# Kernel optimization log

Hardware: AMD Instinct MI355X
Metric: run time of the kernel (lower is better)

## Reference

```python
import jax, jax.numpy as jnp
import numpy as np

N = 50000        # nodes
E = 800000       # edges (avg degree 16)
F = 64           # in/out feature dim (scatter into zeros_like(x) forces out==in)
H = 128          # hidden dim
CIN = 2 * F + 1  # combined_features dim


def setup_inputs() -> dict:
    key = jax.random.key(0)
    ks = jax.random.split(key, 12)
    x = jax.random.normal(ks[0], (N, F), dtype=jnp.float32)
    pos = jax.random.normal(ks[1], (N, 3), dtype=jnp.float32)
    edge_index = jax.random.randint(ks[2], (2, E), 0, N, dtype=jnp.int64)
    s1 = 1.0 / np.sqrt(CIN)
    s2 = 1.0 / np.sqrt(H)
    W1x = jax.random.uniform(ks[3], (CIN, H), jnp.float32, -s1, s1)
    b1x = jax.random.uniform(ks[4], (H,), jnp.float32, -s1, s1)
    W2x = jax.random.uniform(ks[5], (H, F), jnp.float32, -s2, s2)
    b2x = jax.random.uniform(ks[6], (F,), jnp.float32, -s2, s2)
    W1p = jax.random.uniform(ks[7], (CIN, H), jnp.float32, -s1, s1)
    b1p = jax.random.uniform(ks[8], (H,), jnp.float32, -s1, s1)
    W2p = jax.random.uniform(ks[9], (H, 1), jnp.float32, -s2, s2)
    b2p = jax.random.uniform(ks[10], (1,), jnp.float32, -s2, s2)
    return {"x": x, "pos": pos, "edge_index": edge_index,
            "W1x": W1x, "b1x": b1x, "W2x": W2x, "b2x": b2x,
            "W1p": W1p, "b1p": b1p, "W2p": W2p, "b2p": b2p}


def reference(x, pos, edge_index, W1x, b1x, W2x, b2x, W1p, b1p, W2p, b2p):
    row, col = edge_index[0], edge_index[1]
    rel_pos = pos[row] - pos[col]                              # [E, 3]
    dist_sq = jnp.sum(rel_pos * rel_pos, axis=-1, keepdims=True)  # [E, 1]
    combined = jnp.concatenate([x[row], x[col], dist_sq], axis=-1)  # [E, 2F+1]
    # phi_x: Linear -> SiLU -> Linear
    msg_x = jax.nn.silu(combined @ W1x + b1x) @ W2x + b2x      # [E, F]
    aggregated_x = jax.ops.segment_sum(msg_x, col, num_segments=x.shape[0])
    # phi_pos: Linear -> SiLU -> Linear (scalar weight per edge)
    weight_pos = jax.nn.silu(combined @ W1p + b1p) @ W2p + b2p  # [E, 1]
    pos_update = weight_pos * rel_pos                           # [E, 3]
    aggregated_pos = jax.ops.segment_sum(pos_update, col, num_segments=pos.shape[0])
    return aggregated_x, aggregated_pos
```

## Files before the change

### kernel.cpp

```cpp
#include <hip/hip_runtime.h>

typedef short short8 __attribute__((ext_vector_type(8)));
typedef float floatx4 __attribute__((ext_vector_type(4)));

__device__ __forceinline__ unsigned short f2bf(float f) {
  unsigned int u = __float_as_uint(f);
  u += 0x7FFFu + ((u >> 16) & 1u);
  return (unsigned short)(u >> 16);
}

#if __has_builtin(__builtin_amdgcn_cvt_pk_bf16_f32)
typedef __bf16 bf16x2_t __attribute__((ext_vector_type(2)));
__device__ __forceinline__ unsigned int pk2bf(float lo, float hi) {
  bf16x2_t v = __builtin_amdgcn_cvt_pk_bf16_f32(lo, hi);
  return __builtin_bit_cast(unsigned int, v);
}
#else
__device__ __forceinline__ unsigned int pk2bf(float lo, float hi) {
  return (unsigned)f2bf(lo) | ((unsigned)f2bf(hi) << 16);
}
#endif

__device__ __forceinline__ float silu(float h) {
  return h * __builtin_amdgcn_rcpf(1.f + __expf(-h));
}

__global__ __launch_bounds__(256) void k_mega(
    float* __restrict__ out, int out_n,
    const int* __restrict__ colp, int E, int* __restrict__ hist,
    const float* __restrict__ x, int N,
    const float* __restrict__ W1x, const float* __restrict__ W1p,
    const float* __restrict__ W2x,
    const float* __restrict__ b1x, const float* __restrict__ b1p,
    unsigned short* __restrict__ wbuf,
    unsigned int* __restrict__ Ar, unsigned int* __restrict__ Ac,
    int b1, int b2, int b3)
{
  __shared__ __align__(16) unsigned short xt[64][72];
  const int blk = blockIdx.x, t = threadIdx.x;

  if (blk < b1) {
    const int n0 = blk * 64;
    const int wv = t >> 6, lane = t & 63, quad = lane >> 4, lc = lane & 15;

    {
      int nd = t >> 2, p = t & 3;
      int n = n0 + nd;
      uint4 o0, o1;
      if (n < N) {
        const float4* xp = (const float4*)(x + (size_t)n*64 + p*16);
        float4 a = xp[0], b = xp[1], c = xp[2], d = xp[3];
        o0 = make_uint4(pk2bf(a.x,a.y), pk2bf(a.z,a.w), pk2bf(b.x,b.y), pk2bf(b.z,b.w));
        o1 = make_uint4(pk2bf(c.x,c.y), pk2bf(c.z,c.w), pk2bf(d.x,d.y), pk2bf(d.z,d.w));
      } else {
        o0 = o1 = make_uint4(0u,0u,0u,0u);
      }
      *(uint4*)&xt[nd][p*16]     = o0;
      *(uint4*)&xt[nd][p*16 + 8] = o1;
    }

    short8 fxr[2][2], fxc[2][2], fpr[2][2], fpc[2][2];
    float bxv[2][4], bpv[2][4];
    #pragma unroll
    for (int ti = 0; ti < 2; ++ti) {
      const int nt = wv + 4*ti;
      const int n  = nt*16 + lc;
      #pragma unroll
      for (int k2 = 0; k2 < 2; ++k2) {
        #pragma unroll
        for (int j = 0; j < 8; ++j) {
          const int kr = k2*32 + quad*8 + j;
          fxr[ti][k2][j] = (short)f2bf(W1x[kr*128 + n]);
          fxc[ti][k2][j] = (short)f2bf(W1x[(64 + kr)*128 + n]);
          fpr[ti][k2][j] = (short)f2bf(W1p[kr*128 + n]);
          fpc[ti][k2][j] = (short)f2bf(W1p[(64 + kr)*128 + n]);
        }
      }
      #pragma unroll
      for (int r = 0; r < 4; ++r) {
        bxv[ti][r] = b1x[nt*16 + quad*4 + r];
        bpv[ti][r] = b1p[nt*16 + quad*4 + r];
      }
    }
    __syncthreads();

    #pragma unroll 1
    for (int mw = 0; mw < 4; ++mw) {
      short8 bb0 = *(const short8*)&xt[mw*16 + lc][quad*8];
      short8 bb1 = *(const short8*)&xt[mw*16 + lc][32 + quad*8];
      const int nd = n0 + mw*16 + lc;
      #pragma unroll
      for (int ti = 0; ti < 2; ++ti) {
        floatx4 xr = {0,0,0,0}, xc = {0,0,0,0}, pr = {0,0,0,0}, pc = {0,0,0,0};
        xr = __builtin_amdgcn_mfma_f32_16x16x32_bf16(fxr[ti][0], bb0, xr, 0,0,0);
        xr = __builtin_amdgcn_mfma_f32_16x16x32_bf16(fxr[ti][1], bb1, xr, 0,0,0);
        xc = __builtin_amdgcn_mfma_f32_16x16x32_bf16(fxc[ti][0], bb0, xc, 0,0,0);
        xc = __builtin_amdgcn_mfma_f32_16x16x32_bf16(fxc[ti][1], bb1, xc, 0,0,0);
        pr = __builtin_amdgcn_mfma_f32_16x16x32_bf16(fpr[ti][0], bb0, pr, 0,0,0);
        pr = __builtin_amdgcn_mfma_f32_16x16x32_bf16(fpr[ti][1], bb1, pr, 0,0,0);
        pc = __builtin_amdgcn_mfma_f32_16x16x32_bf16(fpc[ti][0], bb0, pc, 0,0,0);
        pc = __builtin_amdgcn_mfma_f32_16x16x32_bf16(fpc[ti][1], bb1, pc, 0,0,0);
        if (nd < N) {
          const int hbase = (wv + 4*ti)*16 + quad*4;
          uint4 ur = make_uint4(pk2bf(xr[0]+bxv[ti][0], pr[0]+bpv[ti][0]),
                                pk2bf(xr[1]+bxv[ti][1], pr[1]+bpv[ti][1]),
                                pk2bf(xr[2]+bxv[ti][2], pr[2]+bpv[ti][2]),
                                pk2bf(xr[3]+bxv[ti][3], pr[3]+bpv[ti][3]));
          uint4 uc = make_uint4(pk2bf(xc[0], pc[0]), pk2bf(xc[1], pc[1]),
                                pk2bf(xc[2], pc[2]), pk2bf(xc[3], pc[3]));
          *(uint4*)(Ar + (size_t)nd*128 + hbase) = ur;
          *(uint4*)(Ac + (size_t)nd*128 + hbase) = uc;
        }
      }
    }
  } else if (blk < b2) {
    int i = ((blk - b1) * 256 + t) * 16;
    #pragma unroll
    for (int q = 0; q < 4; ++q) {
      int j = i + q*4;
      if (j + 4 <= out_n) *(float4*)(out + j) = make_float4(0.f,0.f,0.f,0.f);
      else for (int k = j; k < out_n; ++k) out[k] = 0.f;
    }
  } else if (blk < b3) {
    int i4 = (blk - b2) * 256 + t;
    if (i4 < (E >> 2)) {
      int4 c = *(const int4*)(colp + i4*4);
      atomicAdd(&hist[c.x], 1); atomicAdd(&hist[c.y], 1);
      atomicAdd(&hist[c.z], 1); atomicAdd(&hist[c.w], 1);
    }
    if (blk == b2 && t == 0)
      for (int k = E & ~3; k < E; ++k) atomicAdd(&hist[colp[k]], 1);
  } else {
    int i = (blk - b3) * 256 + t;
    if (i < 8192) {
      int jj = i & 7, lane = (i >> 3) & 63, ks = (i >> 9) & 3, nt = (i >> 11) & 3;
      int k = ks*32 + (lane >> 4)*8 + jj;
      wbuf[i] = f2bf(W2x[k*64 + nt*16 + (lane & 15)]);
    }
  }
}

__global__ __launch_bounds__(256) void k_scan_a(
    int* __restrict__ hist, int N, int* __restrict__ bsum) {
  __shared__ int wtot[4], wexc[4];
  int t = threadIdx.x, lane = t & 63, w = t >> 6;
  int base = blockIdx.x * 1024 + t * 4;
  int v0 = (base + 0 < N) ? hist[base + 0] : 0;
  int v1 = (base + 1 < N) ? hist[base + 1] : 0;
  int v2 = (base + 2 < N) ? hist[base + 2] : 0;
  int v3 = (base + 3 < N) ? hist[base + 3] : 0;
  int T = v0 + v1 + v2 + v3;
  int inc = T;
  #pragma unroll
  for (int s = 1; s < 64; s <<= 1) {
    int u = __shfl_up(inc, s, 64);
    if (lane >= s) inc += u;
  }
  if (lane == 63) wtot[w] = inc;
  __syncthreads();
  if (t == 0) {
    int a = 0;
    #pragma unroll
    for (int i = 0; i < 4; ++i) { wexc[i] = a; a += wtot[i]; }
    bsum[blockIdx.x] = a;
  }
  __syncthreads();
  int tex = wexc[w] + (inc - T);
  if (base + 0 < N) hist[base + 0] = tex;
  if (base + 1 < N) hist[base + 1] = tex + v0;
  if (base + 2 < N) hist[base + 2] = tex + v0 + v1;
  if (base + 3 < N) hist[base + 3] = tex + v0 + v1 + v2;
}

__global__ __launch_bounds__(256) void k_scatter(
    const int* __restrict__ row, const int* __restrict__ col, int E,
    int* __restrict__ excl, const int* __restrict__ bsum, int NB,
    int2* __restrict__ sedge) {
  __shared__ int boff_sh[64];
  int t = threadIdx.x;
  if (t < 64) {
    int v = (t < NB) ? bsum[t] : 0;
    int inc = v;
    #pragma unroll
    for (int s = 1; s < 64; s <<= 1) {
      int u = __shfl_up(inc, s, 64);
      if (t >= s) inc += u;
    }
    boff_sh[t] = inc - v;
  }
  __syncthreads();
  int i4 = blockIdx.x * 256 + t;
  if (i4 < (E >> 2)) {
    int4 c = *(const int4*)(col + i4*4);
    int4 r = *(const int4*)(row + i4*4);
    int p;
    p = atomicAdd(&excl[c.x], 1) + boff_sh[c.x >> 10]; sedge[p] = make_int2(r.x, c.x);
    p = atomicAdd(&excl[c.y], 1) + boff_sh[c.y >> 10]; sedge[p] = make_int2(r.y, c.y);
    p = atomicAdd(&excl[c.z], 1) + boff_sh[c.z >> 10]; sedge[p] = make_int2(r.z, c.z);
    p = atomicAdd(&excl[c.w], 1) + boff_sh[c.w >> 10]; sedge[p] = make_int2(r.w, c.w);
  }
  if (blockIdx.x == 0 && t == 0) {
    for (int k = E & ~3; k < E; ++k) {
      int c = col[k];
      int p = atomicAdd(&excl[c], 1) + boff_sh[c >> 10];
      sedge[p] = make_int2(row[k], c);
    }
  }
}

__global__ __launch_bounds__(256) void mp_main(
    const float* __restrict__ pos,
    const int2* __restrict__ sedge, int E,
    const unsigned int* __restrict__ Ar, const unsigned int* __restrict__ Ac,
    const float* __restrict__ W1x, const float* __restrict__ W1p,
    const float* __restrict__ b2x, const float* __restrict__ W2p,
    const float* __restrict__ b2p,
    const unsigned short* __restrict__ wbuf,
    float* __restrict__ out_x, float* __restrict__ out_pos)
{
  __shared__ __align__(16) unsigned short H_lds[64][136];
  __shared__ __align__(16) uint4 edata[64];
  __shared__ float rel_lds[64][3];
  __shared__ int   col_sh[64];
  __shared__ float wsum[4][64];

  const int t    = threadIdx.x;
  const int e0   = blockIdx.x * 64;
  const int wv   = t >> 6;
  const int lane = t & 63;
  const int quad = lane >> 4;
  const int lc   = lane & 15;

  if (t < 64) {
    int e = e0 + t;
    int r = 0, c = 0, cs = -1;
    float rp0 = 0.f, rp1 = 0.f, rp2 = 0.f, dsq = 0.f;
    if (e < E) {
      int2 rc = sedge[e]; r = rc.x; c = rc.y;
      cs = c;
      float pr0 = pos[r*3+0], pr1 = pos[r*3+1], pr2 = pos[r*3+2];
      float pc0 = pos[c*3+0], pc1 = pos[c*3+1], pc2 = pos[c*3+2];
      rp0 = pr0 - pc0; rp1 = pr1 - pc1; rp2 = pr2 - pc2;
      dsq = rp0*rp0 + rp1*rp1 + rp2*rp2;
    }
    rel_lds[t][0] = rp0; rel_lds[t][1] = rp1; rel_lds[t][2] = rp2;
    col_sh[t] = cs;
    edata[t] = make_uint4((unsigned)r, (unsigned)c, __float_as_uint(dsq), 0u);
  }

  const short8* __restrict__ w2x_f = (const short8*)wbuf;
  short8 a2w[4];
  #pragma unroll
  for (int ks = 0; ks < 4; ++ks) a2w[ks] = w2x_f[(wv*4 + ks)*64 + lane];

  float w1xd[2][4], w1pd[2][4], wp2[2][4], b2xr[4];
  #pragma unroll
  for (int ti = 0; ti < 2; ++ti)
    #pragma unroll
    for (int r = 0; r < 4; ++r) {
      int h = (wv + 4*ti)*16 + quad*4 + r;
      w1xd[ti][r] = W1x[16384 + h];
      w1pd[ti][r] = W1p[16384 + h];
      wp2[ti][r]  = W2p[h];
    }
  #pragma unroll
  for (int r = 0; r < 4; ++r) b2xr[r] = b2x[wv*16 + quad*4 + r];
  const float b2ps = b2p[0];
  __syncthreads();

  #pragma unroll 2
  for (int et = 0; et < 4; ++et) {
    uint4 ed = edata[et*16 + lc];
    const float dsqv = __uint_as_float(ed.z);
    float ps = 0.f;
    #pragma unroll
    for (int ti = 0; ti < 2; ++ti) {
      const int ht = wv + 4*ti;
      const int hb = ht*32 + quad*8;
      uint4 va = *(const uint4*)((const unsigned short*)Ar + (size_t)ed.x*256 + hb);
      uint4 vc = *(const uint4*)((const unsigned short*)Ac + (size_t)ed.y*256 + hb);
      float sx[4];
      #pragma unroll
      for (int j = 0; j < 4; ++j) {
        unsigned a = (&va.x)[j], bb = (&vc.x)[j];
        float hx = __uint_as_float(a << 16) + __uint_as_float(bb << 16)
                 + dsqv * w1xd[ti][j];
        float hp = __uint_as_float(a & 0xffff0000u) + __uint_as_float(bb & 0xffff0000u)
                 + dsqv * w1pd[ti][j];
        sx[j] = silu(hx);
        ps += silu(hp) * wp2[ti][j];
      }
      *(uint2*)&H_lds[et*16 + lc][ht*16 + quad*4] =
          make_uint2(pk2bf(sx[0], sx[1]), pk2bf(sx[2], sx[3]));
    }
    ps += __shfl_xor(ps, 16, 64);
    ps += __shfl_xor(ps, 32, 64);
    if (lane < 16) wsum[wv][et*16 + lane] = ps;
  }
  __syncthreads();

  #pragma unroll 2
  for (int et = 0; et < 4; ++et) {
    floatx4 acc = {0,0,0,0};
    #pragma unroll
    for (int ks = 0; ks < 4; ++ks) {
      short8 b = *(const short8*)&H_lds[et*16 + lc][ks*32 + quad*8];
      acc = __builtin_amdgcn_mfma_f32_16x16x32_bf16(a2w[ks], b, acc, 0, 0, 0);
    }
    int edge = et*16 + lc;
    int myc = col_sh[edge];
    float v0 = acc[0] + b2xr[0], v1 = acc[1] + b2xr[1];
    float v2 = acc[2] + b2xr[2], v3 = acc[3] + b2xr[3];
    #pragma unroll
    for (int s = 1; s < 16; s <<= 1) {
      int   nc = __shfl_down(myc, s, 64);
      float n0 = __shfl_down(v0,  s, 64);
      float n1 = __shfl_down(v1,  s, 64);
      float n2 = __shfl_down(v2,  s, 64);
      float n3 = __shfl_down(v3,  s, 64);
      if ((lc + s < 16) && (nc == myc)) { v0 += n0; v1 += n1; v2 += n2; v3 += n3; }
    }
    bool head = (myc >= 0) && (lc == 0 || col_sh[edge-1] != myc);
    if (head) {
      float* dst = out_x + (size_t)myc*64 + wv*16 + quad*4;
      atomicAdd(dst + 0, v0);
      atomicAdd(dst + 1, v1);
      atomicAdd(dst + 2, v2);
      atomicAdd(dst + 3, v3);
    }
  }

  if (t < 64) {
    int c = col_sh[t];
    float w = wsum[0][t] + wsum[1][t] + wsum[2][t] + wsum[3][t] + b2ps;
    float p0 = w * rel_lds[t][0], p1 = w * rel_lds[t][1], p2 = w * rel_lds[t][2];
    #pragma unroll
    for (int s = 1; s < 64; s <<= 1) {
      int   nc = __shfl_down(c,  s, 64);
      float n0 = __shfl_down(p0, s, 64);
      float n1 = __shfl_down(p1, s, 64);
      float n2 = __shfl_down(p2, s, 64);
      if ((t + s < 64) && (nc == c)) { p0 += n0; p1 += n1; p2 += n2; }
    }
    bool head = (c >= 0) && (t == 0 || col_sh[t-1] != c);
    if (head) {
      atomicAdd(&out_pos[(size_t)c*3 + 0], p0);
      atomicAdd(&out_pos[(size_t)c*3 + 1], p1);
      atomicAdd(&out_pos[(size_t)c*3 + 2], p2);
    }
  }
}

extern "C" void kernel_launch(void* const* d_in, const int* in_sizes, int n_in,
                              void* d_out, int out_size, void* d_ws, size_t ws_size,
                              hipStream_t stream) {
  const float* x   = (const float*)d_in[0];
  const float* pos = (const float*)d_in[1];
  const int*   ei  = (const int*)d_in[2];
  const float* W1x = (const float*)d_in[3];
  const float* b1x = (const float*)d_in[4];
  const float* W2x = (const float*)d_in[5];
  const float* b2x = (const float*)d_in[6];
  const float* W1p = (const float*)d_in[7];
  const float* b1p = (const float*)d_in[8];
  const float* W2p = (const float*)d_in[9];
  const float* b2p = (const float*)d_in[10];

  const int E = in_sizes[2] / 2;
  const int N = in_sizes[0] / 64;
  const int* rowp = ei;
  const int* colp = ei + E;
  float* out_x   = (float*)d_out;
  float* out_pos = out_x + (size_t)N * 64;
  const int NB = (N + 1023) / 1024;

  char* ws = (char*)d_ws;
  const size_t tab_one = (size_t)N * 512;
  unsigned int*   Ar   = (unsigned int*)ws;
  unsigned int*   Ac   = (unsigned int*)(ws + tab_one);
  unsigned short* wbuf = (unsigned short*)(ws + 2*tab_one);
  int*  hist  = (int*)(ws + 2*tab_one + 16384);
  int*  bsum  = (int*)(ws + 2*tab_one + 16384 + 200192);
  int2* sedge = (int2*)(ws + 2*tab_one + 16384 + 200192 + 512);

  hipMemsetAsync(hist, 0, (size_t)N * sizeof(int), stream);

  const int nb_node = (N + 63) / 64;
  const int nb_zero = (out_size + 4095) / 4096;
  const int nb_hist = ((E >> 2) + 255) / 256;
  const int nb_rep  = 32;
  const int b1 = nb_node, b2 = b1 + nb_zero, b3 = b2 + nb_hist;
  k_mega<<<b3 + nb_rep, 256, 0, stream>>>(
      (float*)d_out, out_size, colp, E, hist, x, N,
      W1x, W1p, W2x, b1x, b1p, wbuf, Ar, Ac, b1, b2, b3);

  k_scan_a<<<NB, 256, 0, stream>>>(hist, N, bsum);
  k_scatter<<<((E >> 2) + 255) / 256, 256, 0, stream>>>(
      rowp, colp, E, hist, bsum, NB, sedge);

  mp_main<<<(E + 63) / 64, 256, 0, stream>>>(
      pos, sedge, E, Ar, Ac, W1x, W1p, b2x, W2p, b2p, wbuf, out_x, out_pos);
}
```

Baseline: 311.9 us.

## Prefetch all gathered Ar/Ac rows upfront via wave shuffles, drop edata LDS and barrier

Every wave now loads its 64 edges' indices and positions redundantly, then broadcasts row, col and dist_sq with cross-lane shuffles instead of staging them in shared memory behind a barrier. All 16 uint4 gathers from Ar/Ac per thread are issued at once before the compute loop, so the loads can overlap with each other and with the weight loads. The intent is to hide gather latency and remove one __syncthreads. The cost is much higher register pressure (32 extra VGPR-wide uint4 values), which could lower occupancy, plus redundant index and position loads across the four waves.

```diff
diff --git a/kernel.cpp b/kernel.cpp
--- a/kernel.cpp
+++ b/kernel.cpp
@@ -219,7 +219,6 @@
     float* __restrict__ out_x, float* __restrict__ out_pos)
 {
   __shared__ __align__(16) unsigned short H_lds[64][136];
-  __shared__ __align__(16) uint4 edata[64];
   __shared__ float rel_lds[64][3];
   __shared__ int   col_sh[64];
   __shared__ float wsum[4][64];
@@ -231,21 +230,36 @@
   const int quad = lane >> 4;
   const int lc   = lane & 15;
 
-  if (t < 64) {
-    int e = e0 + t;
-    int r = 0, c = 0, cs = -1;
-    float rp0 = 0.f, rp1 = 0.f, rp2 = 0.f, dsq = 0.f;
+  int erow = 0, ecol = 0, cs = -1;
+  float dsq = 0.f, rp0 = 0.f, rp1 = 0.f, rp2 = 0.f;
+  {
+    int e = e0 + lane;
     if (e < E) {
-      int2 rc = sedge[e]; r = rc.x; c = rc.y;
-      cs = c;
-      float pr0 = pos[r*3+0], pr1 = pos[r*3+1], pr2 = pos[r*3+2];
-      float pc0 = pos[c*3+0], pc1 = pos[c*3+1], pc2 = pos[c*3+2];
+      int2 rc = sedge[e];
+      erow = rc.x; ecol = rc.y; cs = ecol;
+      float pr0 = pos[erow*3+0], pr1 = pos[erow*3+1], pr2 = pos[erow*3+2];
+      float pc0 = pos[ecol*3+0], pc1 = pos[ecol*3+1], pc2 = pos[ecol*3+2];
       rp0 = pr0 - pc0; rp1 = pr1 - pc1; rp2 = pr2 - pc2;
       dsq = rp0*rp0 + rp1*rp1 + rp2*rp2;
     }
+  }
+  if (t < 64) {
     rel_lds[t][0] = rp0; rel_lds[t][1] = rp1; rel_lds[t][2] = rp2;
     col_sh[t] = cs;
-    edata[t] = make_uint4((unsigned)r, (unsigned)c, __float_as_uint(dsq), 0u);
+  }
+
+  uint4 va[4][2], vc[4][2];
+  #pragma unroll
+  for (int et = 0; et < 4; ++et) {
+    const int src = et*16 + lc;
+    int r_et = __shfl(erow, src, 64);
+    int c_et = __shfl(ecol, src, 64);
+    #pragma unroll
+    for (int ti = 0; ti < 2; ++ti) {
+      const int hb = (wv + 4*ti)*32 + quad*8;
+      va[et][ti] = *(const uint4*)((const unsigned short*)Ar + (size_t)r_et*256 + hb);
+      vc[et][ti] = *(const uint4*)((const unsigned short*)Ac + (size_t)c_et*256 + hb);
+    }
   }
 
   const short8* __restrict__ w2x_f = (const short8*)wbuf;
@@ -266,23 +280,18 @@
   #pragma unroll
   for (int r = 0; r < 4; ++r) b2xr[r] = b2x[wv*16 + quad*4 + r];
   const float b2ps = b2p[0];
-  __syncthreads();
-
-  #pragma unroll 2
+
+  #pragma unroll
   for (int et = 0; et < 4; ++et) {
-    uint4 ed = edata[et*16 + lc];
-    const float dsqv = __uint_as_float(ed.z);
+    const float dsqv = __shfl(dsq, et*16 + lc, 64);
     float ps = 0.f;
     #pragma unroll
     for (int ti = 0; ti < 2; ++ti) {
       const int ht = wv + 4*ti;
-      const int hb = ht*32 + quad*8;
-      uint4 va = *(const uint4*)((const unsigned short*)Ar + (size_t)ed.x*256 + hb);
-      uint4 vc = *(const uint4*)((const unsigned short*)Ac + (size_t)ed.y*256 + hb);
       float sx[4];
       #pragma unroll
       for (int j = 0; j < 4; ++j) {
-        unsigned a = (&va.x)[j], bb = (&vc.x)[j];
+        unsigned a = (&va[et][ti].x)[j], bb = (&vc[et][ti].x)[j];
         float hx = __uint_as_float(a << 16) + __uint_as_float(bb << 16)
                  + dsqv * w1xd[ti][j];
         float hp = __uint_as_float(a & 0xffff0000u) + __uint_as_float(bb & 0xffff0000u)
```

After: 330.4 us. +6.0%, slower.

## Make each wave own 16 edges end to end, removing LDS staging and barriers

Applied to the files above, without the earlier changes.

The block's work is repartitioned so that each wavefront handles its own 16 edges through the whole pipeline: gather, first layer, SiLU, the MFMA second layer, and the segmented reductions. Hidden activations now stay in registers as MFMA B operands instead of being staged in LDS, and the block-level syncthreads and shared arrays are removed. Each wave now loads all W2x fragments and all 128 hidden columns per edge, and the pos-weight reduction shrinks from 64 lanes to 16-edge segments. The cost is more atomics on out_pos and higher register pressure from holding all gathered rows at once.

```diff
diff --git a/kernel.cpp b/kernel.cpp
--- a/kernel.cpp
+++ b/kernel.cpp
@@ -218,99 +218,83 @@
     const unsigned short* __restrict__ wbuf,
     float* __restrict__ out_x, float* __restrict__ out_pos)
 {
-  __shared__ __align__(16) unsigned short H_lds[64][136];
-  __shared__ __align__(16) uint4 edata[64];
-  __shared__ float rel_lds[64][3];
-  __shared__ int   col_sh[64];
-  __shared__ float wsum[4][64];
-
   const int t    = threadIdx.x;
-  const int e0   = blockIdx.x * 64;
   const int wv   = t >> 6;
   const int lane = t & 63;
   const int quad = lane >> 4;
   const int lc   = lane & 15;
-
-  if (t < 64) {
-    int e = e0 + t;
-    int r = 0, c = 0, cs = -1;
-    float rp0 = 0.f, rp1 = 0.f, rp2 = 0.f, dsq = 0.f;
+  const int e0   = blockIdx.x * 64 + wv * 16;
+
+  int ecol = -1, grow = 0, gcol = 0;
+  float dsq = 0.f, rp0 = 0.f, rp1 = 0.f, rp2 = 0.f;
+  {
+    int e = e0 + lc;
     if (e < E) {
-      int2 rc = sedge[e]; r = rc.x; c = rc.y;
-      cs = c;
-      float pr0 = pos[r*3+0], pr1 = pos[r*3+1], pr2 = pos[r*3+2];
-      float pc0 = pos[c*3+0], pc1 = pos[c*3+1], pc2 = pos[c*3+2];
+      int2 rc = sedge[e];
+      grow = rc.x; gcol = rc.y; ecol = rc.y;
+      float pr0 = pos[grow*3+0], pr1 = pos[grow*3+1], pr2 = pos[grow*3+2];
+      float pc0 = pos[gcol*3+0], pc1 = pos[gcol*3+1], pc2 = pos[gcol*3+2];
       rp0 = pr0 - pc0; rp1 = pr1 - pc1; rp2 = pr2 - pc2;
       dsq = rp0*rp0 + rp1*rp1 + rp2*rp2;
     }
-    rel_lds[t][0] = rp0; rel_lds[t][1] = rp1; rel_lds[t][2] = rp2;
-    col_sh[t] = cs;
-    edata[t] = make_uint4((unsigned)r, (unsigned)c, __float_as_uint(dsq), 0u);
-  }
+  }
+  const int prevc = __shfl(ecol, lane - 1, 64);
+
+  const unsigned int* arow = Ar + (size_t)grow * 128 + quad * 8;
+  const unsigned int* acol = Ac + (size_t)gcol * 128 + quad * 8;
+  uint4 ga[4][2], gc[4][2];
+  #pragma unroll
+  for (int ks = 0; ks < 4; ++ks) {
+    ga[ks][0] = *(const uint4*)(arow + ks*32);
+    ga[ks][1] = *(const uint4*)(arow + ks*32 + 4);
+    gc[ks][0] = *(const uint4*)(acol + ks*32);
+    gc[ks][1] = *(const uint4*)(acol + ks*32 + 4);
+  }
+
+  short8 bfr[4];
+  float ps = 0.f;
+  #pragma unroll
+  for (int ks = 0; ks < 4; ++ks) {
+    const int hb = ks*32 + quad*8;
+    float4 wx0 = *(const float4*)(W1x + 16384 + hb);
+    float4 wx1 = *(const float4*)(W1x + 16384 + hb + 4);
+    float4 wp0 = *(const float4*)(W1p + 16384 + hb);
+    float4 wp1 = *(const float4*)(W1p + 16384 + hb + 4);
+    float4 w20 = *(const float4*)(W2p + hb);
+    float4 w21 = *(const float4*)(W2p + hb + 4);
+    float sx[8];
+    #pragma unroll
+    for (int j = 0; j < 8; ++j) {
+      unsigned a = (j < 4) ? (&ga[ks][0].x)[j] : (&ga[ks][1].x)[j-4];
+      unsigned c = (j < 4) ? (&gc[ks][0].x)[j] : (&gc[ks][1].x)[j-4];
+      float wxd = (j < 4) ? (&wx0.x)[j] : (&wx1.x)[j-4];
+      float wpd = (j < 4) ? (&wp0.x)[j] : (&wp1.x)[j-4];
+      float w2v = (j < 4) ? (&w20.x)[j] : (&w21.x)[j-4];
+      float hx = __uint_as_float(a << 16) + __uint_as_float(c << 16) + dsq * wxd;
+      float hp = __uint_as_float(a & 0xffff0000u) + __uint_as_float(c & 0xffff0000u)
+               + dsq * wpd;
+      sx[j] = silu(hx);
+      ps += silu(hp) * w2v;
+    }
+    uint4 pk = make_uint4(pk2bf(sx[0], sx[1]), pk2bf(sx[2], sx[3]),
+                          pk2bf(sx[4], sx[5]), pk2bf(sx[6], sx[7]));
+    bfr[ks] = __builtin_bit_cast(short8, pk);
+  }
+  ps += __shfl_xor(ps, 16, 64);
+  ps += __shfl_xor(ps, 32, 64);
 
   const short8* __restrict__ w2x_f = (const short8*)wbuf;
-  short8 a2w[4];
   #pragma unroll
-  for (int ks = 0; ks < 4; ++ks) a2w[ks] = w2x_f[(wv*4 + ks)*64 + lane];
-
-  float w1xd[2][4], w1pd[2][4], wp2[2][4], b2xr[4];
-  #pragma unroll
-  for (int ti = 0; ti < 2; ++ti)
-    #pragma unroll
-    for (int r = 0; r < 4; ++r) {
-      int h = (wv + 4*ti)*16 + quad*4 + r;
-      w1xd[ti][r] = W1x[16384 + h];
-      w1pd[ti][r] = W1p[16384 + h];
-      wp2[ti][r]  = W2p[h];
-    }
-  #pragma unroll
-  for (int r = 0; r < 4; ++r) b2xr[r] = b2x[wv*16 + quad*4 + r];
-  const float b2ps = b2p[0];
-  __syncthreads();
-
-  #pragma unroll 2
-  for (int et = 0; et < 4; ++et) {
-    uint4 ed = edata[et*16 + lc];
-    const float dsqv = __uint_as_float(ed.z);
-    float ps = 0.f;
-    #pragma unroll
-    for (int ti = 0; ti < 2; ++ti) {
-      const int ht = wv + 4*ti;
-      const int hb = ht*32 + quad*8;
-      uint4 va = *(const uint4*)((const unsigned short*)Ar + (size_t)ed.x*256 + hb);
-      uint4 vc = *(const uint4*)((const unsigned short*)Ac + (size_t)ed.y*256 + hb);
-      float sx[4];
-      #pragma unroll
-      for (int j = 0; j < 4; ++j) {
-        unsigned a = (&va.x)[j], bb = (&vc.x)[j];
-        float hx = __uint_as_float(a << 16) + __uint_as_float(bb << 16)
-                 + dsqv * w1xd[ti][j];
-        float hp = __uint_as_float(a & 0xffff0000u) + __uint_as_float(bb & 0xffff0000u)
-                 + dsqv * w1pd[ti][j];
-        sx[j] = silu(hx);
-        ps += silu(hp) * wp2[ti][j];
-      }
-      *(uint2*)&H_lds[et*16 + lc][ht*16 + quad*4] =
-          make_uint2(pk2bf(sx[0], sx[1]), pk2bf(sx[2], sx[3]));
-    }
-    ps += __shfl_xor(ps, 16, 64);
-    ps += __shfl_xor(ps, 32, 64);
-    if (lane < 16) wsum[wv][et*16 + lane] = ps;
-  }
-  __syncthreads();
-
-  #pragma unroll 2
-  for (int et = 0; et < 4; ++et) {
+  for (int ft = 0; ft < 4; ++ft) {
     floatx4 acc = {0,0,0,0};
     #pragma unroll
-    for (int ks = 0; ks < 4; ++ks) {
-      short8 b = *(const short8*)&H_lds[et*16 + lc][ks*32 + quad*8];
-      acc = __builtin_amdgcn_mfma_f32_16x16x32_bf16(a2w[ks], b, acc, 0, 0, 0);
-    }
-    int edge = et*16 + lc;
-    int myc = col_sh[edge];
-    float v0 = acc[0] + b2xr[0], v1 = acc[1] + b2xr[1];
-    float v2 = acc[2] + b2xr[2], v3 = acc[3] + b2xr[3];
+    for (int ks = 0; ks < 4; ++ks)
+      acc = __builtin_amdgcn_mfma_f32_16x16x32_bf16(
+                w2x_f[(ft*4 + ks)*64 + lane], bfr[ks], acc, 0, 0, 0);
+    const float4 b2v = *(const float4*)(b2x + ft*16 + quad*4);
+    int myc = ecol;
+    float v0 = acc[0] + b2v.x, v1 = acc[1] + b2v.y;
+    float v2 = acc[2] + b2v.z, v3 = acc[3] + b2v.w;
     #pragma unroll
     for (int s = 1; s < 16; s <<= 1) {
       int   nc = __shfl_down(myc, s, 64);
@@ -320,9 +304,9 @@
       float n3 = __shfl_down(v3,  s, 64);
       if ((lc + s < 16) && (nc == myc)) { v0 += n0; v1 += n1; v2 += n2; v3 += n3; }
     }
-    bool head = (myc >= 0) && (lc == 0 || col_sh[edge-1] != myc);
+    bool head = (myc >= 0) && (lc == 0 || prevc != myc);
     if (head) {
-      float* dst = out_x + (size_t)myc*64 + wv*16 + quad*4;
+      float* dst = out_x + (size_t)myc*64 + ft*16 + quad*4;
       atomicAdd(dst + 0, v0);
       atomicAdd(dst + 1, v1);
       atomicAdd(dst + 2, v2);
@@ -330,19 +314,19 @@
     }
   }
 
-  if (t < 64) {
-    int c = col_sh[t];
-    float w = wsum[0][t] + wsum[1][t] + wsum[2][t] + wsum[3][t] + b2ps;
-    float p0 = w * rel_lds[t][0], p1 = w * rel_lds[t][1], p2 = w * rel_lds[t][2];
-    #pragma unroll
-    for (int s = 1; s < 64; s <<= 1) {
+  {
+    float w  = ps + b2p[0];
+    float p0 = w * rp0, p1 = w * rp1, p2 = w * rp2;
+    int   c  = ecol;
+    #pragma unroll
+    for (int s = 1; s < 16; s <<= 1) {
       int   nc = __shfl_down(c,  s, 64);
       float n0 = __shfl_down(p0, s, 64);
       float n1 = __shfl_down(p1, s, 64);
       float n2 = __shfl_down(p2, s, 64);
-      if ((t + s < 64) && (nc == c)) { p0 += n0; p1 += n1; p2 += n2; }
-    }
-    bool head = (c >= 0) && (t == 0 || col_sh[t-1] != c);
+      if ((lc + s < 16) && (nc == c)) { p0 += n0; p1 += n1; p2 += n2; }
+    }
+    bool head = (c >= 0) && (quad == 0) && (lc == 0 || prevc != c);
     if (head) {
       atomicAdd(&out_pos[(size_t)c*3 + 0], p0);
       atomicAdd(&out_pos[(size_t)c*3 + 1], p1);
```

Measured after the change: 326.3 us. +4.6%, slower.
